# Kernel optimization log

Hardware: AMD Instinct MI355X
Metric: run time of the kernel (lower is better)

Reference implementation:

```python
import jax, jax.numpy as jnp
import numpy as np

H = 10   # GRU hidden size
L = 10   # num layers
E = 400  # embedding dim
V = 100000
T, B = 84, 96


def gru_layer(x, w_ih, w_hh, b_ih, b_hh, reverse):
    # x: (T, B, in_dim); w_ih: (3H, in_dim); w_hh: (3H, H)
    xp = jnp.einsum('tbi,gi->tbg', x, w_ih) + b_ih  # (T, B, 3H)
    if reverse:
        xp = xp[::-1]

    def step(h, xt):
        gh = h @ w_hh.T + b_hh
        xr, xz, xn = jnp.split(xt, 3, axis=-1)
        hr, hz, hn = jnp.split(gh, 3, axis=-1)
        r = jax.nn.sigmoid(xr + hr)
        z = jax.nn.sigmoid(xz + hz)
        n = jnp.tanh(xn + r * hn)
        h_new = (1.0 - z) * n + z * h
        return h_new, h_new

    h0 = jnp.zeros((x.shape[1], H), x.dtype)
    _, ys = jax.lax.scan(step, h0, xp)
    if reverse:
        ys = ys[::-1]
    return ys  # (T, B, H)


def setup_inputs():
    key = jax.random.key(0)
    ks = jax.random.split(key, 12)
    s = 0.05
    return {
        'x': jax.random.randint(ks[0], (T, B), 0, V),
        'emb': jax.random.normal(ks[1], (V, E), jnp.float32) * 0.1,
        'w_ih0': jax.random.normal(ks[2], (2, 3 * H, E), jnp.float32) * s,
        'w_hh0': jax.random.normal(ks[3], (2, 3 * H, H), jnp.float32) * s,
        'b_ih0': jax.random.normal(ks[4], (2, 3 * H), jnp.float32) * s,
        'b_hh0': jax.random.normal(ks[5], (2, 3 * H), jnp.float32) * s,
        'w_ih': jax.random.normal(ks[6], (L - 1, 2, 3 * H, 2 * H), jnp.float32) * s,
        'w_hh': jax.random.normal(ks[7], (L - 1, 2, 3 * H, H), jnp.float32) * s,
        'b_ih': jax.random.normal(ks[8], (L - 1, 2, 3 * H), jnp.float32) * s,
        'b_hh': jax.random.normal(ks[9], (L - 1, 2, 3 * H), jnp.float32) * s,
        'lin_w': jax.random.normal(ks[10], (19, 336), jnp.float32) * s,
        'lin_b': jax.random.normal(ks[11], (19,), jnp.float32) * s,
    }


def reference(x, emb, w_ih0, w_hh0, b_ih0, b_hh0, w_ih, w_hh, b_ih, b_hh, lin_w, lin_b):
    out = emb[x]  # (T, B, 400)
    for l in range(L):
        if l == 0:
            wi, wh, bi, bh = w_ih0, w_hh0, b_ih0, b_hh0
        else:
            wi, wh, bi, bh = w_ih[l - 1], w_hh[l - 1], b_ih[l - 1], b_hh[l - 1]
        fwd = gru_layer(out, wi[0], wh[0], bi[0], bh[0], False)
        bwd = gru_layer(out, wi[1], wh[1], bi[1], bh[1], True)
        out = jnp.concatenate([fwd, bwd], axis=-1)  # (T, B, 20)
        # dropout p=0.2 between layers is disabled (eval-mode reference)
    # AvgPool2d(3)/MaxPool2d(3) on 3D input pool over (batch, feature) dims
    trimmed = out[:, : (B // 3) * 3, :18].reshape(T, B // 3, 3, 6, 3)
    avg = trimmed.mean(axis=(2, 4))  # (T, B//3, 6)
    mx = trimmed.max(axis=(2, 4))    # (T, B//3, 6)
    cat = jnp.concatenate([avg, mx], axis=2)  # (T, B//3, 12)
    flat = cat.reshape(-1, 336)  # (96, 336)
    # dropout p=0.2 disabled (eval-mode reference)
    return jax.nn.sigmoid(flat @ lin_w.T + lin_b)
```

## Files before the change

kernel.cpp:

```cpp
#include <hip/hip_runtime.h>
#include <math.h>

#define TT 84
#define BB 96
#define GB 6
#define NG 16
#define NTOK (TT*BB)
#define RW4 6

#define S_RZ (-1.4426950408889634f)
#define S_N  (-2.8853900817779268f)

__device__ __forceinline__ float frcp(float x)  { return __builtin_amdgcn_rcpf(x); }
__device__ __forceinline__ float fexp2(float x) { return __builtin_amdgcn_exp2f(x); }

__global__ __launch_bounds__(256) void proj0_kernel(
    const int* __restrict__ x, const float* __restrict__ emb,
    const float* __restrict__ wih0, const float* __restrict__ bih0,
    float* __restrict__ xp, unsigned int* __restrict__ bar)
{
    if (blockIdx.x == 0 && threadIdx.x == 0) bar[0] = 0u;
    __shared__ float4 xrow[32][100];
    const int tok0 = blockIdx.x * 32;
    for (int u = threadIdx.x; u < 32*100; u += 256) {
        int tk = u / 100, i4 = u % 100;
        int row = x[tok0 + tk];
        xrow[tk][i4] = ((const float4*)emb)[row*100 + i4];
    }
    __syncthreads();
    const int g64 = threadIdx.x & 63;
    const int q   = threadIdx.x >> 6;
    if (g64 >= 60) return;
    const int dir = g64 / 30, gg = g64 % 30;
    const float sc = (gg < 20) ? S_RZ : S_N;
    const float bias = bih0[dir*30 + gg];
    float acc[8];
    #pragma unroll
    for (int c = 0; c < 8; ++c) acc[c] = bias;
    const float4* w4 = ((const float4*)wih0) + (dir*30 + gg)*100;
    for (int i4 = 0; i4 < 100; ++i4) {
        float4 w = w4[i4];
        #pragma unroll
        for (int c = 0; c < 8; ++c) {
            float4 xv = xrow[q*8 + c][i4];
            acc[c] += w.x*xv.x + w.y*xv.y + w.z*xv.z + w.w*xv.w;
        }
    }
    #pragma unroll
    for (int c = 0; c < 8; ++c) {
        int tok = tok0 + q*8 + c;
        int t = tok / BB, b = tok % BB;
        xp[((size_t)((dir*TT + t)*BB + b))*30 + gg] = acc[c]*sc;
    }
}

__device__ __forceinline__ float gru_cell(
    float xr, float xz, float xn,
    float4 ha, float4 hb, float4 hc,
    const float* wr, const float* wz, const float* wn,
    float bhr, float bhz, float bhn, float& hown)
{
    float hr0 = fmaf(wr[0], ha.x, bhr), hr1 = wr[1]*ha.y;
    float hz0 = fmaf(wz[0], ha.x, bhz), hz1 = wz[1]*ha.y;
    float hn0 = fmaf(wn[0], ha.x, bhn), hn1 = wn[1]*ha.y;
    hr0 = fmaf(wr[2], ha.z, hr0); hr1 = fmaf(wr[3], ha.w, hr1);
    hz0 = fmaf(wz[2], ha.z, hz0); hz1 = fmaf(wz[3], ha.w, hz1);
    hn0 = fmaf(wn[2], ha.z, hn0); hn1 = fmaf(wn[3], ha.w, hn1);
    hr0 = fmaf(wr[4], hb.x, hr0); hr1 = fmaf(wr[5], hb.y, hr1);
    hz0 = fmaf(wz[4], hb.x, hz0); hz1 = fmaf(wz[5], hb.y, hz1);
    hn0 = fmaf(wn[4], hb.x, hn0); hn1 = fmaf(wn[5], hb.y, hn1);
    hr0 = fmaf(wr[6], hb.z, hr0); hr1 = fmaf(wr[7], hb.w, hr1);
    hz0 = fmaf(wz[6], hb.z, hz0); hz1 = fmaf(wz[7], hb.w, hz1);
    hn0 = fmaf(wn[6], hb.z, hn0); hn1 = fmaf(wn[7], hb.w, hn1);
    hr0 = fmaf(wr[8], hc.x, hr0); hr1 = fmaf(wr[9], hc.y, hr1);
    hz0 = fmaf(wz[8], hc.x, hz0); hz1 = fmaf(wz[9], hc.y, hz1);
    hn0 = fmaf(wn[8], hc.x, hn0); hn1 = fmaf(wn[9], hc.y, hn1);
    float r = frcp(1.f + fexp2(xr + hr0 + hr1));
    float z = frcp(1.f + fexp2(xz + hz0 + hz1));
    float an = fmaf(r, hn0 + hn1, xn);
    float n  = fmaf(2.f, frcp(1.f + fexp2(an)), -1.f);
    float hnew = n + z*(hown - n);
    hown = hnew;
    return hnew;
}

__device__ __forceinline__ void proj20(
    const float4* A, const float* wpr, const float* wpz, const float* wpn,
    float bir, float biz, float bin, float& xr, float& xz, float& xn)
{
    float a[24];
    #pragma unroll
    for (int q = 0; q < 6; ++q) {
        a[4*q]=A[q].x; a[4*q+1]=A[q].y; a[4*q+2]=A[q].z; a[4*q+3]=A[q].w;
    }
    xr = bir; xz = biz; xn = bin;
    #pragma unroll
    for (int c = 0; c < 20; ++c) {
        float av = a[c + (c >= 10 ? 2 : 0)];
        xr = fmaf(wpr[c], av, xr); xz = fmaf(wpz[c], av, xz); xn = fmaf(wpn[c], av, xn);
    }
}

template<bool LAST>
__device__ __forceinline__ void gru_mid(
    const float* __restrict__ wi, const float* __restrict__ bi,
    const float* __restrict__ wh, const float* __restrict__ bh,
    const float4* in4, float4* out4, float* __restrict__ actG,
    int bl, int j, bool act_ln, int b, int dir, int dt, int t0)
{
    float wpr[20], wpz[20], wpn[20];
    {
        const float4* p0 = (const float4*)(wi + j*20);
        const float4* p1 = (const float4*)(wi + (10+j)*20);
        const float4* p2 = (const float4*)(wi + (20+j)*20);
        #pragma unroll
        for (int q = 0; q < 5; ++q) {
            float4 a = p0[q]; wpr[4*q]=a.x*S_RZ; wpr[4*q+1]=a.y*S_RZ; wpr[4*q+2]=a.z*S_RZ; wpr[4*q+3]=a.w*S_RZ;
            float4 c = p1[q]; wpz[4*q]=c.x*S_RZ; wpz[4*q+1]=c.y*S_RZ; wpz[4*q+2]=c.z*S_RZ; wpz[4*q+3]=c.w*S_RZ;
            float4 d = p2[q]; wpn[4*q]=d.x*S_N;  wpn[4*q+1]=d.y*S_N;  wpn[4*q+2]=d.z*S_N;  wpn[4*q+3]=d.w*S_N;
        }
    }
    const float bir = bi[j]*S_RZ, biz = bi[10+j]*S_RZ, bin = bi[20+j]*S_N;
    float wr[10], wz[10], wn[10];
    {
        const float2* p0 = (const float2*)(wh + j*10);
        const float2* p1 = (const float2*)(wh + (10+j)*10);
        const float2* p2 = (const float2*)(wh + (20+j)*10);
        #pragma unroll
        for (int q = 0; q < 5; ++q) {
            float2 a = p0[q]; wr[2*q]=a.x*S_RZ; wr[2*q+1]=a.y*S_RZ;
            float2 c = p1[q]; wz[2*q]=c.x*S_RZ; wz[2*q+1]=c.y*S_RZ;
            float2 d = p2[q]; wn[2*q]=d.x*S_N;  wn[2*q+1]=d.y*S_N;
        }
    }
    const float bhr = bh[j]*S_RZ, bhz = bh[10+j]*S_RZ, bhn = bh[20+j]*S_N;

    float4 ha = {0,0,0,0}, hb = {0,0,0,0}, hc = {0,0,0,0};
    float hown = 0.f;
    float4 A[6], B[6];
    float xr_c, xz_c, xn_c, xr_n, xz_n, xn_n;
    int t = t0;
    {
        const float4* p0 = &in4[(t0*GB + bl)*RW4];
        #pragma unroll
        for (int q = 0; q < 6; ++q) B[q] = p0[q];
        const float4* p1 = &in4[((t0 + dt)*GB + bl)*RW4];
        #pragma unroll
        for (int q = 0; q < 6; ++q) A[q] = p1[q];
        proj20(B, wpr, wpz, wpn, bir, biz, bin, xr_c, xz_c, xn_c);
    }

    #pragma unroll 1
    for (int s = 0; s < TT; s += 2) {
        {
            float hnew = gru_cell(xr_c, xz_c, xn_c, ha, hb, hc, wr, wz, wn, bhr, bhz, bhn, hown);
            ((float*)&out4[(t*GB + bl)*RW4])[dir*12 + j] = hnew;
            const float4* hr = &out4[(t*GB + bl)*RW4 + dir*3];
            ha = hr[0]; hb = hr[1]; hc = hr[2];
            __builtin_amdgcn_sched_barrier(0);
            if (LAST && act_ln) actG[(size_t)(t*BB + b)*20 + dir*10 + j] = hnew;
            int tl = t + 2*dt; tl = tl < 0 ? 0 : (tl > TT-1 ? TT-1 : tl);
            const float4* pl = &in4[(tl*GB + bl)*RW4];
            #pragma unroll
            for (int q = 0; q < 6; ++q) B[q] = pl[q];
            proj20(A, wpr, wpz, wpn, bir, biz, bin, xr_n, xz_n, xn_n);
            t += dt;
        }
        {
            float hnew = gru_cell(xr_n, xz_n, xn_n, ha, hb, hc, wr, wz, wn, bhr, bhz, bhn, hown);
            ((float*)&out4[(t*GB + bl)*RW4])[dir*12 + j] = hnew;
            const float4* hr = &out4[(t*GB + bl)*RW4 + dir*3];
            ha = hr[0]; hb = hr[1]; hc = hr[2];
            __builtin_amdgcn_sched_barrier(0);
            if (LAST && act_ln) actG[(size_t)(t*BB + b)*20 + dir*10 + j] = hnew;
            int tl = t + 2*dt; tl = tl < 0 ? 0 : (tl > TT-1 ? TT-1 : tl);
            const float4* pl = &in4[(tl*GB + bl)*RW4];
            #pragma unroll
            for (int q = 0; q < 6; ++q) A[q] = pl[q];
            proj20(B, wpr, wpz, wpn, bir, biz, bin, xr_c, xz_c, xn_c);
            t += dt;
        }
    }
}

__global__ __launch_bounds__(128, 1) void mega_kernel(
    const float* __restrict__ xp0,
    const float* __restrict__ whh0, const float* __restrict__ bhh0,
    const float* __restrict__ wih,  const float* __restrict__ bih,
    const float* __restrict__ whh,  const float* __restrict__ bhh,
    const float* __restrict__ lin_w, const float* __restrict__ lin_b,
    float* __restrict__ actG, unsigned int* __restrict__ bar,
    float* __restrict__ out)
{
    __shared__ float4 actA4[TT*GB*RW4];
    __shared__ float4 actB4[TT*GB*RW4];

    const int tid  = threadIdx.x;
    const int dir  = tid >> 6;
    const int lane = tid & 63;
    int bl = lane / 10; if (bl > 5) bl = 5;
    int j  = lane - bl*10; if (j > 9) j = 9;
    const bool act_ln = (lane < 60);
    const int grp = blockIdx.x;
    const int b   = grp*GB + bl;
    const int dt  = dir ? -1 : 1;
    const int t0  = dir ? TT-1 : 0;

    {
        float wr[10], wz[10], wn[10];
        const float* wh = whh0 + dir*300;
        {
            const float2* p0 = (const float2*)(wh + j*10);
            const float2* p1 = (const float2*)(wh + (10+j)*10);
            const float2* p2 = (const float2*)(wh + (20+j)*10);
            #pragma unroll
            for (int q = 0; q < 5; ++q) {
                float2 a = p0[q]; wr[2*q]=a.x*S_RZ; wr[2*q+1]=a.y*S_RZ;
                float2 c = p1[q]; wz[2*q]=c.x*S_RZ; wz[2*q+1]=c.y*S_RZ;
                float2 d = p2[q]; wn[2*q]=d.x*S_N;  wn[2*q+1]=d.y*S_N;
            }
        }
        const float bhr = bhh0[dir*30 + j]*S_RZ;
        const float bhz = bhh0[dir*30 + 10 + j]*S_RZ;
        const float bhn = bhh0[dir*30 + 20 + j]*S_N;

        float4 ha = {0,0,0,0}, hb = {0,0,0,0}, hc = {0,0,0,0};
        float hown = 0.f;
        int t = t0;
        const float* xb = xp0 + (size_t)dir*TT*BB*30;

        float xr_c = xb[(size_t)(t*BB + b)*30 + j];
        float xz_c = xb[(size_t)(t*BB + b)*30 + 10 + j];
        float xn_c = xb[(size_t)(t*BB + b)*30 + 20 + j];

        #pragma unroll 1
        for (int s = 0; s < TT; ++s) {
            float hnew = gru_cell(xr_c, xz_c, xn_c, ha, hb, hc, wr, wz, wn, bhr, bhz, bhn, hown);
            ((float*)&actA4[(t*GB + bl)*RW4])[dir*12 + j] = hnew;
            const float4* hr = &actA4[(t*GB + bl)*RW4 + dir*3];
            ha = hr[0]; hb = hr[1]; hc = hr[2];
            __builtin_amdgcn_sched_barrier(0);
            int tn = (s == TT-1) ? t : t + dt;
            xr_c = xb[(size_t)(tn*BB + b)*30 + j];
            xz_c = xb[(size_t)(tn*BB + b)*30 + 10 + j];
            xn_c = xb[(size_t)(tn*BB + b)*30 + 20 + j];
            t = tn;
        }
    }
    __syncthreads();

    #pragma unroll 1
    for (int lp = 0; lp < 4; ++lp) {
        int l = 1 + lp*2;
        gru_mid<false>(wih + (size_t)((l-1)*2 + dir)*600, bih + (size_t)((l-1)*2 + dir)*30,
                       whh + (size_t)((l-1)*2 + dir)*300, bhh + (size_t)((l-1)*2 + dir)*30,
                       actA4, actB4, actG, bl, j, act_ln, b, dir, dt, t0);
        __syncthreads();
        l = 2 + lp*2;
        gru_mid<false>(wih + (size_t)((l-1)*2 + dir)*600, bih + (size_t)((l-1)*2 + dir)*30,
                       whh + (size_t)((l-1)*2 + dir)*300, bhh + (size_t)((l-1)*2 + dir)*30,
                       actB4, actA4, actG, bl, j, act_ln, b, dir, dt, t0);
        __syncthreads();
    }
    gru_mid<true>(wih + (size_t)(8*2 + dir)*600, bih + (size_t)(8*2 + dir)*30,
                  whh + (size_t)(8*2 + dir)*300, bhh + (size_t)(8*2 + dir)*30,
                  actA4, actB4, actG, bl, j, act_ln, b, dir, dt, t0);

    __threadfence();
    __syncthreads();
    if (tid == 0) {
        __hip_atomic_fetch_add(bar, 1u, __ATOMIC_ACQ_REL, __HIP_MEMORY_SCOPE_AGENT);
        while (__hip_atomic_load(bar, __ATOMIC_ACQUIRE, __HIP_MEMORY_SCOPE_AGENT) < (unsigned)NG)
            __builtin_amdgcn_s_sleep(1);
    }
    __syncthreads();
    __threadfence();

    float* feat = (float*)actA4;
    for (int u = tid; u < GB*336; u += 128) {
        int q = u / 336, v = u % 336;
        int r = grp*GB + q;
        int qq = v / 12, f = v % 12;
        int pair = r*28 + qq;
        int t = pair / 32, bb = pair % 32;
        int jj = (f < 6) ? f : f - 6;
        float acc = (f < 6) ? 0.f : -1e30f;
        #pragma unroll
        for (int i = 0; i < 3; ++i) {
            #pragma unroll
            for (int kk = 0; kk < 3; ++kk) {
                float vv = actG[(size_t)(t*BB + bb*3 + i)*20 + jj*3 + kk];
                if (f < 6) acc += vv; else acc = fmaxf(acc, vv);
            }
        }
        feat[u] = (f < 6) ? acc*(1.f/9.f) : acc;
    }
    __syncthreads();
    if (tid < GB*19) {
        int q = tid / 19, o = tid % 19;
        int r = grp*GB + q;
        float acc = lin_b[o];
        const float* wrow = lin_w + o*336;
        const float* frow = feat + q*336;
        for (int v = 0; v < 336; ++v) acc = fmaf(frow[v], wrow[v], acc);
        out[r*19 + o] = frcp(1.f + __expf(-acc));
    }
}

extern "C" void kernel_launch(void* const* d_in, const int* in_sizes, int n_in,
                              void* d_out, int out_size, void* d_ws, size_t ws_size,
                              hipStream_t stream)
{
    const int*   x     = (const int*)  d_in[0];
    const float* emb   = (const float*)d_in[1];
    const float* wih0  = (const float*)d_in[2];
    const float* whh0  = (const float*)d_in[3];
    const float* bih0  = (const float*)d_in[4];
    const float* bhh0  = (const float*)d_in[5];
    const float* wih   = (const float*)d_in[6];
    const float* whh   = (const float*)d_in[7];
    const float* bih   = (const float*)d_in[8];
    const float* bhh   = (const float*)d_in[9];
    const float* lin_w = (const float*)d_in[10];
    const float* lin_b = (const float*)d_in[11];
    float* out = (float*)d_out;

    float* xp0  = (float*)d_ws;
    float* actG = xp0 + (size_t)2*NTOK*30;
    unsigned int* bar = (unsigned int*)(actG + (size_t)NTOK*20);

    proj0_kernel<<<252, 256, 0, stream>>>(x, emb, wih0, bih0, xp0, bar);
    mega_kernel<<<NG, 128, 0, stream>>>(xp0, whh0, bhh0, wih, bih, whh, bhh,
                                        lin_w, lin_b, actG, bar, out);
}
```

Baseline: 486.1 us.

## Hoist per-layer input projection out of the recurrent scan into a parallel phase

Each layer's input-to-hidden projection is no longer computed inside the sequential scan loop. After each layer's scan, all 256 threads compute the next layer's projections over all timesteps in parallel and write them to the global xp buffer, which the scan then reads with a two-step prefetch. This removes the 20-wide dot products from the serial recurrence path and drops the second LDS activation buffer. The cost is extra global memory traffic, an extra barrier per layer, and global-load latency in the scan loop.

Result: faster. 473.9 us (-2.5%).

```diff
diff --git a/kernel.cpp b/kernel.cpp
--- a/kernel.cpp
+++ b/kernel.cpp
@@ -101,26 +101,12 @@
     }
 }
 
-template<bool LAST>
-__device__ __forceinline__ void gru_mid(
-    const float* __restrict__ wi, const float* __restrict__ bi,
-    const float* __restrict__ wh, const float* __restrict__ bh,
-    const float4* in4, float4* out4, float* __restrict__ actG,
+__device__ __forceinline__ void scan_layer(
+    const float* __restrict__ xb,
+    const float* __restrict__ wh, const float* __restrict__ bh3,
+    float4* __restrict__ act4, float* __restrict__ actG, bool last,
     int bl, int j, bool act_ln, int b, int dir, int dt, int t0)
 {
-    float wpr[20], wpz[20], wpn[20];
-    {
-        const float4* p0 = (const float4*)(wi + j*20);
-        const float4* p1 = (const float4*)(wi + (10+j)*20);
-        const float4* p2 = (const float4*)(wi + (20+j)*20);
-        #pragma unroll
-        for (int q = 0; q < 5; ++q) {
-            float4 a = p0[q]; wpr[4*q]=a.x*S_RZ; wpr[4*q+1]=a.y*S_RZ; wpr[4*q+2]=a.z*S_RZ; wpr[4*q+3]=a.w*S_RZ;
-            float4 c = p1[q]; wpz[4*q]=c.x*S_RZ; wpz[4*q+1]=c.y*S_RZ; wpz[4*q+2]=c.z*S_RZ; wpz[4*q+3]=c.w*S_RZ;
-            float4 d = p2[q]; wpn[4*q]=d.x*S_N;  wpn[4*q+1]=d.y*S_N;  wpn[4*q+2]=d.z*S_N;  wpn[4*q+3]=d.w*S_N;
-        }
-    }
-    const float bir = bi[j]*S_RZ, biz = bi[10+j]*S_RZ, bin = bi[20+j]*S_N;
     float wr[10], wz[10], wn[10];
     {
         const float2* p0 = (const float2*)(wh + j*10);
@@ -133,58 +119,37 @@
             float2 d = p2[q]; wn[2*q]=d.x*S_N;  wn[2*q+1]=d.y*S_N;
         }
     }
-    const float bhr = bh[j]*S_RZ, bhz = bh[10+j]*S_RZ, bhn = bh[20+j]*S_N;
+    const float bhr = bh3[j]*S_RZ, bhz = bh3[10+j]*S_RZ, bhn = bh3[20+j]*S_N;
 
     float4 ha = {0,0,0,0}, hb = {0,0,0,0}, hc = {0,0,0,0};
     float hown = 0.f;
-    float4 A[6], B[6];
-    float xr_c, xz_c, xn_c, xr_n, xz_n, xn_n;
     int t = t0;
-    {
-        const float4* p0 = &in4[(t0*GB + bl)*RW4];
-        #pragma unroll
-        for (int q = 0; q < 6; ++q) B[q] = p0[q];
-        const float4* p1 = &in4[((t0 + dt)*GB + bl)*RW4];
-        #pragma unroll
-        for (int q = 0; q < 6; ++q) A[q] = p1[q];
-        proj20(B, wpr, wpz, wpn, bir, biz, bin, xr_c, xz_c, xn_c);
-    }
+    float xr0 = xb[(size_t)(t0*BB + b)*30 + j];
+    float xz0 = xb[(size_t)(t0*BB + b)*30 + 10 + j];
+    float xn0 = xb[(size_t)(t0*BB + b)*30 + 20 + j];
+    const int t1 = t0 + dt;
+    float xr1 = xb[(size_t)(t1*BB + b)*30 + j];
+    float xz1 = xb[(size_t)(t1*BB + b)*30 + 10 + j];
+    float xn1 = xb[(size_t)(t1*BB + b)*30 + 20 + j];
 
     #pragma unroll 1
-    for (int s = 0; s < TT; s += 2) {
-        {
-            float hnew = gru_cell(xr_c, xz_c, xn_c, ha, hb, hc, wr, wz, wn, bhr, bhz, bhn, hown);
-            ((float*)&out4[(t*GB + bl)*RW4])[dir*12 + j] = hnew;
-            const float4* hr = &out4[(t*GB + bl)*RW4 + dir*3];
-            ha = hr[0]; hb = hr[1]; hc = hr[2];
-            __builtin_amdgcn_sched_barrier(0);
-            if (LAST && act_ln) actG[(size_t)(t*BB + b)*20 + dir*10 + j] = hnew;
-            int tl = t + 2*dt; tl = tl < 0 ? 0 : (tl > TT-1 ? TT-1 : tl);
-            const float4* pl = &in4[(tl*GB + bl)*RW4];
-            #pragma unroll
-            for (int q = 0; q < 6; ++q) B[q] = pl[q];
-            proj20(A, wpr, wpz, wpn, bir, biz, bin, xr_n, xz_n, xn_n);
-            t += dt;
-        }
-        {
-            float hnew = gru_cell(xr_n, xz_n, xn_n, ha, hb, hc, wr, wz, wn, bhr, bhz, bhn, hown);
-            ((float*)&out4[(t*GB + bl)*RW4])[dir*12 + j] = hnew;
-            const float4* hr = &out4[(t*GB + bl)*RW4 + dir*3];
-            ha = hr[0]; hb = hr[1]; hc = hr[2];
-            __builtin_amdgcn_sched_barrier(0);
-            if (LAST && act_ln) actG[(size_t)(t*BB + b)*20 + dir*10 + j] = hnew;
-            int tl = t + 2*dt; tl = tl < 0 ? 0 : (tl > TT-1 ? TT-1 : tl);
-            const float4* pl = &in4[(tl*GB + bl)*RW4];
-            #pragma unroll
-            for (int q = 0; q < 6; ++q) A[q] = pl[q];
-            proj20(B, wpr, wpz, wpn, bir, biz, bin, xr_c, xz_c, xn_c);
-            t += dt;
-        }
-    }
-}
-
-__global__ __launch_bounds__(128, 1) void mega_kernel(
-    const float* __restrict__ xp0,
+    for (int s = 0; s < TT; ++s) {
+        float hnew = gru_cell(xr0, xz0, xn0, ha, hb, hc, wr, wz, wn, bhr, bhz, bhn, hown);
+        ((float*)&act4[(t*GB + bl)*RW4])[dir*12 + j] = hnew;
+        const float4* hr = &act4[(t*GB + bl)*RW4 + dir*3];
+        ha = hr[0]; hb = hr[1]; hc = hr[2];
+        __builtin_amdgcn_sched_barrier(0);
+        if (last && act_ln) actG[(size_t)(t*BB + b)*20 + dir*10 + j] = hnew;
+        int tp = t + 2*dt; tp = tp < 0 ? 0 : (tp > TT-1 ? TT-1 : tp);
+        xr0 = xr1; xz0 = xz1; xn0 = xn1;
+        const float* px = xb + (size_t)(tp*BB + b)*30;
+        xr1 = px[j]; xz1 = px[10 + j]; xn1 = px[20 + j];
+        t += dt;
+    }
+}
+
+__global__ __launch_bounds__(256, 1) void mega_kernel(
+    float* __restrict__ xp,
     const float* __restrict__ whh0, const float* __restrict__ bhh0,
     const float* __restrict__ wih,  const float* __restrict__ bih,
     const float* __restrict__ whh,  const float* __restrict__ bhh,
@@ -192,79 +157,67 @@
     float* __restrict__ actG, unsigned int* __restrict__ bar,
     float* __restrict__ out)
 {
-    __shared__ float4 actA4[TT*GB*RW4];
-    __shared__ float4 actB4[TT*GB*RW4];
+    __shared__ float4 act4[TT*GB*RW4];
 
     const int tid  = threadIdx.x;
-    const int dir  = tid >> 6;
+    const int grp  = blockIdx.x;
+
+    const int dir  = (tid >> 6) & 1;
     const int lane = tid & 63;
     int bl = lane / 10; if (bl > 5) bl = 5;
     int j  = lane - bl*10; if (j > 9) j = 9;
     const bool act_ln = (lane < 60);
-    const int grp = blockIdx.x;
-    const int b   = grp*GB + bl;
-    const int dt  = dir ? -1 : 1;
-    const int t0  = dir ? TT-1 : 0;
-
-    {
-        float wr[10], wz[10], wn[10];
-        const float* wh = whh0 + dir*300;
-        {
-            const float2* p0 = (const float2*)(wh + j*10);
-            const float2* p1 = (const float2*)(wh + (10+j)*10);
-            const float2* p2 = (const float2*)(wh + (20+j)*10);
-            #pragma unroll
-            for (int q = 0; q < 5; ++q) {
-                float2 a = p0[q]; wr[2*q]=a.x*S_RZ; wr[2*q+1]=a.y*S_RZ;
-                float2 c = p1[q]; wz[2*q]=c.x*S_RZ; wz[2*q+1]=c.y*S_RZ;
-                float2 d = p2[q]; wn[2*q]=d.x*S_N;  wn[2*q+1]=d.y*S_N;
+    const int b  = grp*GB + bl;
+    const int dt = dir ? -1 : 1;
+    const int t0 = dir ? TT-1 : 0;
+
+    const int half = tid / 120;
+    const int prr  = tid % 120;
+    const int dp   = prr / 60;
+    const int prr2 = prr % 60;
+    const int blp  = prr2 / 10;
+    const int jp   = prr2 % 10;
+
+    #pragma unroll 1
+    for (int l = 0; l < 10; ++l) {
+        if (tid < 128) {
+            const float* wh  = (l == 0) ? (whh0 + dir*300)
+                                        : (whh + (size_t)((l-1)*2 + dir)*300);
+            const float* bh3 = (l == 0) ? (bhh0 + dir*30)
+                                        : (bhh + (size_t)((l-1)*2 + dir)*30);
+            scan_layer(xp + (size_t)dir*TT*BB*30, wh, bh3, act4, actG, (l == 9),
+                       bl, j, act_ln, b, dir, dt, t0);
+        }
+        __syncthreads();
+        if (l < 9) {
+            if (tid < 240) {
+                const float* wi = wih + (size_t)(l*2 + dp)*600;
+                const float* bi = bih + (size_t)(l*2 + dp)*30;
+                float wpr[20], wpz[20], wpn[20];
+                {
+                    const float4* p0 = (const float4*)(wi + jp*20);
+                    const float4* p1 = (const float4*)(wi + (10+jp)*20);
+                    const float4* p2 = (const float4*)(wi + (20+jp)*20);
+                    #pragma unroll
+                    for (int q = 0; q < 5; ++q) {
+                        float4 a = p0[q]; wpr[4*q]=a.x*S_RZ; wpr[4*q+1]=a.y*S_RZ; wpr[4*q+2]=a.z*S_RZ; wpr[4*q+3]=a.w*S_RZ;
+                        float4 c = p1[q]; wpz[4*q]=c.x*S_RZ; wpz[4*q+1]=c.y*S_RZ; wpz[4*q+2]=c.z*S_RZ; wpz[4*q+3]=c.w*S_RZ;
+                        float4 d = p2[q]; wpn[4*q]=d.x*S_N;  wpn[4*q+1]=d.y*S_N;  wpn[4*q+2]=d.z*S_N;  wpn[4*q+3]=d.w*S_N;
+                    }
+                }
+                const float bir = bi[jp]*S_RZ, biz = bi[10+jp]*S_RZ, bin = bi[20+jp]*S_N;
+                const int bg = grp*GB + blp;
+                #pragma unroll 1
+                for (int t = half*(TT/2); t < (half+1)*(TT/2); ++t) {
+                    float xr, xz, xn;
+                    proj20(&act4[(t*GB + blp)*RW4], wpr, wpz, wpn, bir, biz, bin, xr, xz, xn);
+                    float* px = xp + ((size_t)(dp*TT + t)*BB + bg)*30;
+                    px[jp] = xr; px[10+jp] = xz; px[20+jp] = xn;
+                }
             }
-        }
-        const float bhr = bhh0[dir*30 + j]*S_RZ;
-        const float bhz = bhh0[dir*30 + 10 + j]*S_RZ;
-        const float bhn = bhh0[dir*30 + 20 + j]*S_N;
-
-        float4 ha = {0,0,0,0}, hb = {0,0,0,0}, hc = {0,0,0,0};
-        float hown = 0.f;
-        int t = t0;
-        const float* xb = xp0 + (size_t)dir*TT*BB*30;
-
-        float xr_c = xb[(size_t)(t*BB + b)*30 + j];
-        float xz_c = xb[(size_t)(t*BB + b)*30 + 10 + j];
-        float xn_c = xb[(size_t)(t*BB + b)*30 + 20 + j];
-
-        #pragma unroll 1
-        for (int s = 0; s < TT; ++s) {
-            float hnew = gru_cell(xr_c, xz_c, xn_c, ha, hb, hc, wr, wz, wn, bhr, bhz, bhn, hown);
-            ((float*)&actA4[(t*GB + bl)*RW4])[dir*12 + j] = hnew;
-            const float4* hr = &actA4[(t*GB + bl)*RW4 + dir*3];
-            ha = hr[0]; hb = hr[1]; hc = hr[2];
-            __builtin_amdgcn_sched_barrier(0);
-            int tn = (s == TT-1) ? t : t + dt;
-            xr_c = xb[(size_t)(tn*BB + b)*30 + j];
-            xz_c = xb[(size_t)(tn*BB + b)*30 + 10 + j];
-            xn_c = xb[(size_t)(tn*BB + b)*30 + 20 + j];
-            t = tn;
-        }
-    }
-    __syncthreads();
-
-    #pragma unroll 1
-    for (int lp = 0; lp < 4; ++lp) {
-        int l = 1 + lp*2;
-        gru_mid<false>(wih + (size_t)((l-1)*2 + dir)*600, bih + (size_t)((l-1)*2 + dir)*30,
-                       whh + (size_t)((l-1)*2 + dir)*300, bhh + (size_t)((l-1)*2 + dir)*30,
-                       actA4, actB4, actG, bl, j, act_ln, b, dir, dt, t0);
-        __syncthreads();
-        l = 2 + lp*2;
-        gru_mid<false>(wih + (size_t)((l-1)*2 + dir)*600, bih + (size_t)((l-1)*2 + dir)*30,
-                       whh + (size_t)((l-1)*2 + dir)*300, bhh + (size_t)((l-1)*2 + dir)*30,
-                       actB4, actA4, actG, bl, j, act_ln, b, dir, dt, t0);
-        __syncthreads();
-    }
-    gru_mid<true>(wih + (size_t)(8*2 + dir)*600, bih + (size_t)(8*2 + dir)*30,
-                  whh + (size_t)(8*2 + dir)*300, bhh + (size_t)(8*2 + dir)*30,
-                  actA4, actB4, actG, bl, j, act_ln, b, dir, dt, t0);
+            __syncthreads();
+        }
+    }
 
     __threadfence();
     __syncthreads();
@@ -276,8 +229,8 @@
     __syncthreads();
     __threadfence();
 
-    float* feat = (float*)actA4;
-    for (int u = tid; u < GB*336; u += 128) {
+    float* feat = (float*)act4;
+    for (int u = tid; u < GB*336; u += 256) {
         int q = u / 336, v = u % 336;
         int r = grp*GB + q;
         int qq = v / 12, f = v % 12;
@@ -330,6 +283,6 @@
     unsigned int* bar = (unsigned int*)(actG + (size_t)NTOK*20);
 
     proj0_kernel<<<252, 256, 0, stream>>>(x, emb, wih0, bih0, xp0, bar);
-    mega_kernel<<<NG, 128, 0, stream>>>(xp0, whh0, bhh0, wih, bih, whh, bhh,
+    mega_kernel<<<NG, 256, 0, stream>>>(xp0, whh0, bhh0, wih, bih, whh, bhh,
                                         lin_w, lin_b, actG, bar, out);
 }
```
